# Kernel tuning notes

Measured on AMD Instinct MI355X. Metric: run time of the kernel, lower is better.

Reference implementation:

```python
import jax, jax.numpy as jnp
import numpy as np

N = 100000
E = 3200000
IN_C = 1433
DIM = 32
HEADS = 8
OUT_C = 4
NUM_LAYER = 2
NUM_CLASS = 7
NEG_SLOPE = 0.2


def setup_inputs() -> dict:
    key = jax.random.key(0)
    ks = jax.random.split(key, 12)
    s = 0.05
    return {
        "x": jax.random.normal(ks[0], (N, IN_C), dtype=jnp.float32),
        "edge_index": jax.random.randint(ks[1], (2, E), 0, N, dtype=jnp.int32),
        "w_proj": jax.random.normal(ks[2], (IN_C, DIM), dtype=jnp.float32) * s,
        "b_proj": jnp.zeros((DIM,), dtype=jnp.float32),
        "w_l": jax.random.normal(ks[3], (NUM_LAYER, DIM, HEADS * OUT_C), dtype=jnp.float32) * s,
        "b_l": jnp.zeros((NUM_LAYER, HEADS * OUT_C), dtype=jnp.float32),
        "w_r": jax.random.normal(ks[4], (NUM_LAYER, DIM, HEADS * OUT_C), dtype=jnp.float32) * s,
        "b_r": jnp.zeros((NUM_LAYER, HEADS * OUT_C), dtype=jnp.float32),
        "att": jax.random.normal(ks[5], (NUM_LAYER, HEADS, OUT_C), dtype=jnp.float32) * s,
        "conv_bias": jnp.zeros((NUM_LAYER, HEADS * OUT_C), dtype=jnp.float32),
        "w_pred": jax.random.normal(ks[6], (DIM, NUM_CLASS), dtype=jnp.float32) * s,
        "b_pred": jnp.zeros((NUM_CLASS,), dtype=jnp.float32),
    }


def _gatv2_layer(h, src, dst, wl, bl, wr, br, att, bias):
    # GATv2 (PyG semantics): x_l from source, x_r from target,
    # e = att . leaky_relu(x_l[src] + x_r[dst]); softmax over edges per dst.
    xl = (h @ wl + bl).reshape(N, HEADS, OUT_C)
    xr = (h @ wr + br).reshape(N, HEADS, OUT_C)
    e = jax.nn.leaky_relu(xl[src] + xr[dst], NEG_SLOPE)          # [E, H, C]
    logits = jnp.einsum("ehc,hc->eh", e, att)                    # [E, H]
    m = jax.ops.segment_max(logits, dst, num_segments=N)         # [N, H]
    m = jnp.where(jnp.isfinite(m), m, 0.0)                       # empty segments
    ex = jnp.exp(logits - m[dst])                                # [E, H]
    denom = jax.ops.segment_sum(ex, dst, num_segments=N)         # [N, H]
    alpha = ex / jnp.maximum(denom[dst], 1e-16)                  # [E, H]
    msg = alpha[:, :, None] * xl[src]                            # [E, H, C]
    out = jax.ops.segment_sum(msg, dst, num_segments=N)          # [N, H, C]
    return out.reshape(N, HEADS * OUT_C) + bias


def reference(x, edge_index, w_proj, b_proj, w_l, b_l, w_r, b_r, att, conv_bias, w_pred, b_pred):
    src = edge_index[0]
    dst = edge_index[1]
    h = x @ w_proj + b_proj                                      # [N, DIM]
    for i in range(NUM_LAYER):
        h = h + _gatv2_layer(h, src, dst, w_l[i], b_l[i], w_r[i], b_r[i], att[i], conv_bias[i])
    return h @ w_pred + b_pred                                   # [N, NUM_CLASS]
```

## Files before the change

kernel.cpp:

```cpp
#include <hip/hip_runtime.h>

#define N_NODES 100000
#define N_EDGES 3200000
#define IN_C 1433
#define DIM 32
#define HEADS 8
#define OUT_C 4
#define NUM_CLASS 7

#define KTILES 45
#define N_WAVES 6250
#define PROJ_BLOCKS 1563
#define NB_SCAN 98

typedef __bf16 bf16x8 __attribute__((ext_vector_type(8)));
typedef __bf16 bf16x4 __attribute__((ext_vector_type(4)));
typedef float f32x4 __attribute__((ext_vector_type(4)));

__global__ __launch_bounds__(256) void init_kernel(
    const float* __restrict__ w, const float* __restrict__ wl0,
    const float* __restrict__ wr0,
    bf16x8* __restrict__ wfrag, bf16x8* __restrict__ wfrag2,
    int* __restrict__ cnt) {
  const int g = blockIdx.x * 256 + threadIdx.x;
  if (g < N_NODES) cnt[g] = 0;
  if (blockIdx.x < KTILES * 2 && threadIdx.x < 64) {
    const int kt = blockIdx.x >> 1;
    const int ch = blockIdx.x & 1;
    const int l = threadIdx.x;
    const int col = ch * 16 + (l & 15);
    const int kbase = kt * 32 + (l >> 4) * 8;
    bf16x8 v;
    #pragma unroll
    for (int e = 0; e < 8; ++e) {
      const int k = kbase + e;
      v[e] = (__bf16)((k < IN_C) ? w[(size_t)k * DIM + col] : 0.f);
    }
    wfrag[(size_t)blockIdx.x * 64 + l] = v;
  } else if (blockIdx.x < KTILES * 2 + 4 && threadIdx.x < 64) {
    const int bf = blockIdx.x - KTILES * 2;
    const float* ws = (bf < 2) ? wl0 : wr0;
    const int ch = bf & 1;
    const int l = threadIdx.x;
    const int col = ch * 16 + (l & 15);
    const int kbase = (l >> 4) * 8;
    bf16x8 v;
    #pragma unroll
    for (int e = 0; e < 8; ++e)
      v[e] = (__bf16)ws[(size_t)(kbase + e) * DIM + col];
    wfrag2[(size_t)bf * 64 + l] = v;
  }
}

__global__ __launch_bounds__(256) void proj_count_kernel(
    const float* __restrict__ x, const bf16x8* __restrict__ wfrag,
    const bf16x8* __restrict__ wfrag2,
    const float* __restrict__ b, const float* __restrict__ bl0,
    const float* __restrict__ br0, float* __restrict__ h,
    __bf16* __restrict__ xlbA, float* __restrict__ xrA,
    const int* __restrict__ dst, int* __restrict__ cnt,
    int* __restrict__ rank) {
  __shared__ float stage[4][16 * 32];
  const int t = threadIdx.x;
  const int lane = t & 63;
  const int wid = t >> 6;
  const int widx = blockIdx.x * 4 + wid;

  if (widx < N_WAVES) {
    const int nodeBase = widx * 16;
    float* slab = stage[wid];

    const int qrow = lane >> 3;
    const int qcol = lane & 7;
    const float* xq = x + (size_t)(nodeBase + qrow) * IN_C + qcol * 4;

    const int frow = lane & 15;
    const int kg = lane >> 4;
    const int sw = frow & 7;
    const int rd0 = frow * 32 + (((2 * kg) ^ sw) << 2);
    const int rd1 = frow * 32 + (((2 * kg + 1) ^ sw) << 2);
    const bf16x8* wp = wfrag + lane;

    f32x4 acc0 = {0.f, 0.f, 0.f, 0.f};
    f32x4 acc1 = {0.f, 0.f, 0.f, 0.f};

    f32x4 a0 = *(const f32x4*)(xq);
    f32x4 b0v = *(const f32x4*)(xq + (size_t)8 * IN_C);
    f32x4 a1 = *(const f32x4*)(xq + 32);
    f32x4 b1v = *(const f32x4*)(xq + 32 + (size_t)8 * IN_C);

    for (int kt = 0; kt < KTILES - 1; ++kt) {
      {
        const int g0 = qcol ^ (qrow & 7);
        *(f32x4*)(slab + qrow * 32 + (g0 << 2)) = a0;
        const int r1 = qrow + 8;
        const int g1 = qcol ^ (r1 & 7);
        *(f32x4*)(slab + r1 * 32 + (g1 << 2)) = b0v;
      }
      a0 = a1; b0v = b1v;
      if (kt + 2 < KTILES - 1) {
        const float* xp = xq + (size_t)(kt + 2) * 32;
        a1 = *(const f32x4*)(xp);
        b1v = *(const f32x4*)(xp + (size_t)8 * IN_C);
      }
      const f32x4 lo = *(const f32x4*)(slab + rd0);
      const f32x4 hi = *(const f32x4*)(slab + rd1);
      bf16x8 af;
      af[0] = (__bf16)lo[0]; af[1] = (__bf16)lo[1];
      af[2] = (__bf16)lo[2]; af[3] = (__bf16)lo[3];
      af[4] = (__bf16)hi[0]; af[5] = (__bf16)hi[1];
      af[6] = (__bf16)hi[2]; af[7] = (__bf16)hi[3];
      const bf16x8 b0 = wp[(kt * 2 + 0) * 64];
      const bf16x8 b1 = wp[(kt * 2 + 1) * 64];
      acc0 = __builtin_amdgcn_mfma_f32_16x16x32_bf16(af, b0, acc0, 0, 0, 0);
      acc1 = __builtin_amdgcn_mfma_f32_16x16x32_bf16(af, b1, acc1, 0, 0, 0);
    }
    {
      const int srow = lane >> 5;
      const int scol = lane & 31;
      const bool ok = (1408 + scol) < IN_C;
      const float* xt = x + (size_t)(nodeBase + srow) * IN_C + 1408 + scol;
      #pragma unroll
      for (int i = 0; i < 8; ++i) {
        const int row = 2 * i + srow;
        const float v = ok ? xt[(size_t)(2 * i) * IN_C] : 0.f;
        const int p = (scol >> 2) ^ (row & 7);
        slab[row * 32 + (p << 2) + (scol & 3)] = v;
      }
      const f32x4 lo = *(const f32x4*)(slab + rd0);
      const f32x4 hi = *(const f32x4*)(slab + rd1);
      bf16x8 af;
      af[0] = (__bf16)lo[0]; af[1] = (__bf16)lo[1];
      af[2] = (__bf16)lo[2]; af[3] = (__bf16)lo[3];
      af[4] = (__bf16)hi[0]; af[5] = (__bf16)hi[1];
      af[6] = (__bf16)hi[2]; af[7] = (__bf16)hi[3];
      const bf16x8 b0 = wp[((KTILES - 1) * 2 + 0) * 64];
      const bf16x8 b1 = wp[((KTILES - 1) * 2 + 1) * 64];
      acc0 = __builtin_amdgcn_mfma_f32_16x16x32_bf16(af, b0, acc0, 0, 0, 0);
      acc1 = __builtin_amdgcn_mfma_f32_16x16x32_bf16(af, b1, acc1, 0, 0, 0);
    }

    const float bc0 = b[frow];
    const float bc1 = b[frow + 16];
    #pragma unroll
    for (int rg = 0; rg < 4; ++rg) {
      const int nl = kg * 4 + rg;
      const float o0 = acc0[rg] + bc0;
      const float o1 = acc1[rg] + bc1;
      const size_t o = (size_t)(nodeBase + nl) * DIM + frow;
      h[o] = o0;
      h[o + 16] = o1;
      slab[nl * 32 + frow] = o0;
      slab[nl * 32 + frow + 16] = o1;
    }
    {
      const f32x4 lo = *(const f32x4*)(slab + frow * 32 + kg * 8);
      const f32x4 hi = *(const f32x4*)(slab + frow * 32 + kg * 8 + 4);
      bf16x8 af;
      af[0] = (__bf16)lo[0]; af[1] = (__bf16)lo[1];
      af[2] = (__bf16)lo[2]; af[3] = (__bf16)lo[3];
      af[4] = (__bf16)hi[0]; af[5] = (__bf16)hi[1];
      af[6] = (__bf16)hi[2]; af[7] = (__bf16)hi[3];
      f32x4 xl0 = {0.f, 0.f, 0.f, 0.f}, xl1 = {0.f, 0.f, 0.f, 0.f};
      f32x4 xr0 = {0.f, 0.f, 0.f, 0.f}, xr1 = {0.f, 0.f, 0.f, 0.f};
      xl0 = __builtin_amdgcn_mfma_f32_16x16x32_bf16(af, wfrag2[0 * 64 + lane], xl0, 0, 0, 0);
      xl1 = __builtin_amdgcn_mfma_f32_16x16x32_bf16(af, wfrag2[1 * 64 + lane], xl1, 0, 0, 0);
      xr0 = __builtin_amdgcn_mfma_f32_16x16x32_bf16(af, wfrag2[2 * 64 + lane], xr0, 0, 0, 0);
      xr1 = __builtin_amdgcn_mfma_f32_16x16x32_bf16(af, wfrag2[3 * 64 + lane], xr1, 0, 0, 0);
      const float bl_0 = bl0[frow], bl_1 = bl0[frow + 16];
      const float br_0 = br0[frow], br_1 = br0[frow + 16];
      #pragma unroll
      for (int rg = 0; rg < 4; ++rg) {
        const int nl = kg * 4 + rg;
        const size_t o = ((size_t)(nodeBase + nl) << 5) + frow;
        xlbA[o] = (__bf16)(xl0[rg] + bl_0);
        xlbA[o + 16] = (__bf16)(xl1[rg] + bl_1);
        xrA[o] = xr0[rg] + br_0;
        xrA[o + 16] = xr1[rg] + br_1;
      }
    }
  }

  for (int e = blockIdx.x * 256 + t; e < N_EDGES; e += PROJ_BLOCKS * 256)
    rank[e] = atomicAdd(&cnt[dst[e]], 1);
}

__global__ __launch_bounds__(1024) void scan_local_kernel(
    const int* __restrict__ cnt, int* __restrict__ offs, int* __restrict__ bsum) {
  __shared__ int wsum[16];
  const int t = threadIdx.x;
  const int lane = t & 63;
  const int wid = t >> 6;
  const int idx = blockIdx.x * 1024 + t;
  const int v = (idx < N_NODES) ? cnt[idx] : 0;
  int incl = v;
  #pragma unroll
  for (int off = 1; off < 64; off <<= 1) {
    const int nv = __shfl_up(incl, off, 64);
    if (lane >= off) incl += nv;
  }
  if (lane == 63) wsum[wid] = incl;
  __syncthreads();
  int wpre = 0;
  for (int i = 0; i < wid; ++i) wpre += wsum[i];
  if (idx < N_NODES) offs[idx] = wpre + incl - v;
  if (t == 1023) bsum[blockIdx.x] = wpre + incl;
}

__global__ __launch_bounds__(256) void scan_add_kernel(
    int* __restrict__ offs, const int* __restrict__ bsum) {
  __shared__ int wsum[4];
  const int t = threadIdx.x;
  const int lane = t & 63;
  const int wid = t >> 6;
  const int k = blockIdx.x >> 2;
  int v = (t < k) ? bsum[t] : 0;
  #pragma unroll
  for (int m = 1; m < 64; m <<= 1) v += __shfl_xor(v, m, 64);
  if (lane == 0) wsum[wid] = v;
  __syncthreads();
  const int base = wsum[0] + wsum[1] + wsum[2] + wsum[3];
  const int idx = blockIdx.x * 256 + t;
  if (idx < N_NODES) offs[idx] += base;
  if (idx == 0) offs[N_NODES] = N_EDGES;
}

__global__ __launch_bounds__(256) void scatter_kernel(
    const int* __restrict__ src, const int* __restrict__ dst,
    const int* __restrict__ offs, const int* __restrict__ rank,
    int* __restrict__ srcs) {
  const int i = blockIdx.x * 256 + threadIdx.x;
  if (i < N_EDGES) {
    const int d = dst[i];
    srcs[offs[d] + rank[i]] = src[i];
  }
}

__global__ __launch_bounds__(256) void gat_lgemm_kernel(
    const float* __restrict__ hin, const __bf16* __restrict__ xlb,
    const float* __restrict__ xr, const float* __restrict__ att,
    const float* __restrict__ cbias, const int* __restrict__ offs,
    const int* __restrict__ srcs, float* __restrict__ hout,
    const float* __restrict__ wl1, const float* __restrict__ bl1,
    const float* __restrict__ wr1, const float* __restrict__ br1,
    __bf16* __restrict__ xlbB, float* __restrict__ xrB) {
  __shared__ float wls[DIM * DIM];
  __shared__ float wrs[DIM * DIM];
  const int t = threadIdx.x;
  for (int i2 = t; i2 < DIM * DIM; i2 += 256) { wls[i2] = wl1[i2]; wrs[i2] = wr1[i2]; }
  __syncthreads();

  const int lane = t & 63;
  const int node = blockIdx.x * 4 + (t >> 6);
  const int head = lane & 7;
  const int e8 = lane >> 3;
  const float4 a4 = *(const float4*)(att + head * 4);
  const float4 r4 = *(const float4*)(xr + (size_t)node * DIM + head * 4);
  const int beg = offs[node];
  const int end = offs[node + 1];
  float den = 0.f, acc0 = 0.f, acc1 = 0.f, acc2 = 0.f, acc3 = 0.f;
  int i = beg + e8;
  int sNext = (i < end) ? srcs[i] : 0;
  for (; i < end; i += 8) {
    const int s = sNext;
    if (i + 8 < end) sNext = srcs[i + 8];
    const bf16x4 lb = *(const bf16x4*)(xlb + ((size_t)s << 5) + (head << 2));
    const float l0 = (float)lb[0], l1 = (float)lb[1], l2 = (float)lb[2], l3 = (float)lb[3];
    float e0 = l0 + r4.x; e0 = (e0 > 0.f) ? e0 : 0.2f * e0;
    float e1 = l1 + r4.y; e1 = (e1 > 0.f) ? e1 : 0.2f * e1;
    float e2 = l2 + r4.z; e2 = (e2 > 0.f) ? e2 : 0.2f * e2;
    float e3 = l3 + r4.w; e3 = (e3 > 0.f) ? e3 : 0.2f * e3;
    const float logit = e0 * a4.x + e1 * a4.y + e2 * a4.z + e3 * a4.w;
    const float wgt = __expf(logit);
    den += wgt;
    acc0 += wgt * l0; acc1 += wgt * l1; acc2 += wgt * l2; acc3 += wgt * l3;
  }
  #pragma unroll
  for (int m = 8; m <= 32; m <<= 1) {
    den  += __shfl_xor(den, m, 64);
    acc0 += __shfl_xor(acc0, m, 64);
    acc1 += __shfl_xor(acc1, m, 64);
    acc2 += __shfl_xor(acc2, m, 64);
    acc3 += __shfl_xor(acc3, m, 64);
  }
  const float inv = 1.f / fmaxf(den, 1e-16f);
  const int o = node * DIM + head * 4;
  const float4 hv = *(const float4*)(hin + o);
  const float4 cb = *(const float4*)(cbias + head * 4);
  const float o0 = hv.x + cb.x + acc0 * inv;
  const float o1 = hv.y + cb.y + acc1 * inv;
  const float o2 = hv.z + cb.z + acc2 * inv;
  const float o3 = hv.w + cb.w + acc3 * inv;
  if (lane < 8) {
    float4 outv; outv.x = o0; outv.y = o1; outv.z = o2; outv.w = o3;
    *(float4*)(hout + o) = outv;
  }
  const int col = lane & 31;
  const float* wsel = (lane < 32) ? wls : wrs;
  float a = (lane < 32) ? bl1[col] : br1[col];
  #pragma unroll
  for (int k = 0; k < DIM; ++k) {
    const float src = (k & 3) == 0 ? o0 : (k & 3) == 1 ? o1 : (k & 3) == 2 ? o2 : o3;
    const float hk = __shfl(src, k >> 2, 64);
    a += hk * wsel[k * DIM + col];
  }
  const size_t xo = ((size_t)node << 5) + col;
  if (lane < 32) xlbB[xo] = (__bf16)a;
  else           xrB[xo] = a;
}

__global__ __launch_bounds__(256) void gat_edge_pred_kernel(
    const float* __restrict__ hin, const __bf16* __restrict__ xlb,
    const float* __restrict__ xr, const float* __restrict__ att,
    const float* __restrict__ cbias, const int* __restrict__ offs,
    const int* __restrict__ srcs,
    const float* __restrict__ wp, const float* __restrict__ bp,
    float* __restrict__ out) {
  const int t = threadIdx.x;
  const int lane = t & 63;
  const int node = blockIdx.x * 4 + (t >> 6);
  const int head = lane & 7;
  const int e8 = lane >> 3;
  const float4 a4 = *(const float4*)(att + head * 4);
  const float4 r4 = *(const float4*)(xr + (size_t)node * DIM + head * 4);
  const int beg = offs[node];
  const int end = offs[node + 1];
  float den = 0.f, acc0 = 0.f, acc1 = 0.f, acc2 = 0.f, acc3 = 0.f;
  int i = beg + e8;
  int sNext = (i < end) ? srcs[i] : 0;
  for (; i < end; i += 8) {
    const int s = sNext;
    if (i + 8 < end) sNext = srcs[i + 8];
    const bf16x4 lb = *(const bf16x4*)(xlb + ((size_t)s << 5) + (head << 2));
    const float l0 = (float)lb[0], l1 = (float)lb[1], l2 = (float)lb[2], l3 = (float)lb[3];
    float e0 = l0 + r4.x; e0 = (e0 > 0.f) ? e0 : 0.2f * e0;
    float e1 = l1 + r4.y; e1 = (e1 > 0.f) ? e1 : 0.2f * e1;
    float e2 = l2 + r4.z; e2 = (e2 > 0.f) ? e2 : 0.2f * e2;
    float e3 = l3 + r4.w; e3 = (e3 > 0.f) ? e3 : 0.2f * e3;
    const float logit = e0 * a4.x + e1 * a4.y + e2 * a4.z + e3 * a4.w;
    const float wgt = __expf(logit);
    den += wgt;
    acc0 += wgt * l0; acc1 += wgt * l1; acc2 += wgt * l2; acc3 += wgt * l3;
  }
  #pragma unroll
  for (int m = 8; m <= 32; m <<= 1) {
    den  += __shfl_xor(den, m, 64);
    acc0 += __shfl_xor(acc0, m, 64);
    acc1 += __shfl_xor(acc1, m, 64);
    acc2 += __shfl_xor(acc2, m, 64);
    acc3 += __shfl_xor(acc3, m, 64);
  }
  const float inv = 1.f / fmaxf(den, 1e-16f);
  const int o = node * DIM + head * 4;
  const float4 hv = *(const float4*)(hin + o);
  const float4 cb = *(const float4*)(cbias + head * 4);
  const float o0 = hv.x + cb.x + acc0 * inv;
  const float o1 = hv.y + cb.y + acc1 * inv;
  const float o2 = hv.z + cb.z + acc2 * inv;
  const float o3 = hv.w + cb.w + acc3 * inv;
  float pj[NUM_CLASS];
  const float* wr0 = wp + (head * 4 + 0) * NUM_CLASS;
  const float* wr1 = wp + (head * 4 + 1) * NUM_CLASS;
  const float* wr2 = wp + (head * 4 + 2) * NUM_CLASS;
  const float* wr3 = wp + (head * 4 + 3) * NUM_CLASS;
  #pragma unroll
  for (int j = 0; j < NUM_CLASS; ++j)
    pj[j] = o0 * wr0[j] + o1 * wr1[j] + o2 * wr2[j] + o3 * wr3[j];
  #pragma unroll
  for (int m = 1; m <= 4; m <<= 1) {
    #pragma unroll
    for (int j = 0; j < NUM_CLASS; ++j) pj[j] += __shfl_xor(pj[j], m, 64);
  }
  if (lane == 0) {
    #pragma unroll
    for (int j = 0; j < NUM_CLASS; ++j)
      out[(size_t)node * NUM_CLASS + j] = pj[j] + bp[j];
  }
}

extern "C" void kernel_launch(void* const* d_in, const int* in_sizes, int n_in,
                              void* d_out, int out_size, void* d_ws, size_t ws_size,
                              hipStream_t stream) {
  const float* x       = (const float*)d_in[0];
  const int*   ei      = (const int*)d_in[1];
  const float* w_proj  = (const float*)d_in[2];
  const float* b_proj  = (const float*)d_in[3];
  const float* w_l     = (const float*)d_in[4];
  const float* b_l     = (const float*)d_in[5];
  const float* w_r     = (const float*)d_in[6];
  const float* b_r     = (const float*)d_in[7];
  const float* att     = (const float*)d_in[8];
  const float* cbias   = (const float*)d_in[9];
  const float* w_pred  = (const float*)d_in[10];
  const float* b_pred  = (const float*)d_in[11];

  const int* e_src = ei;
  const int* e_dst = ei + N_EDGES;

  char* wsp = (char*)d_ws;
  size_t off = 0;
  auto take = [&](size_t bytes) -> void* {
    void* p = wsp + off;
    off += (bytes + 255) & ~(size_t)255;
    return p;
  };
  float*  h0     = (float*)take((size_t)N_NODES * DIM * 4);
  float*  h1     = (float*)take((size_t)N_NODES * DIM * 4);
  __bf16* xlbA   = (__bf16*)take((size_t)N_NODES * DIM * 2);
  float*  xrA    = (float*)take((size_t)N_NODES * DIM * 4);
  __bf16* xlbB   = (__bf16*)take((size_t)N_NODES * DIM * 2);
  float*  xrB    = (float*)take((size_t)N_NODES * DIM * 4);
  int*    offs   = (int*)take((size_t)(N_NODES + 1) * 4);
  int*    cnt    = (int*)take((size_t)N_NODES * 4);
  int*    bsum   = (int*)take((size_t)NB_SCAN * 4);
  int*    srcs   = (int*)take((size_t)N_EDGES * 4);
  int*    rank   = (int*)take((size_t)N_EDGES * 4);
  bf16x8* wfrag  = (bf16x8*)take((size_t)KTILES * 2 * 64 * 16);
  bf16x8* wfrag2 = (bf16x8*)take((size_t)4 * 64 * 16);

  init_kernel<<<(N_NODES + 255) / 256, 256, 0, stream>>>(
      w_proj, w_l, w_r, wfrag, wfrag2, cnt);
  proj_count_kernel<<<PROJ_BLOCKS, 256, 0, stream>>>(
      x, wfrag, wfrag2, b_proj, b_l, b_r, h0, xlbA, xrA, e_dst, cnt, rank);
  scan_local_kernel<<<NB_SCAN, 1024, 0, stream>>>(cnt, offs, bsum);
  scan_add_kernel<<<(N_NODES + 255) / 256, 256, 0, stream>>>(offs, bsum);
  scatter_kernel<<<(N_EDGES + 255) / 256, 256, 0, stream>>>(
      e_src, e_dst, offs, rank, srcs);
  gat_lgemm_kernel<<<N_NODES / 4, 256, 0, stream>>>(
      h0, xlbA, xrA, att, cbias, offs, srcs, h1,
      w_l + DIM * DIM, b_l + DIM, w_r + DIM * DIM, b_r + DIM, xlbB, xrB);
  gat_edge_pred_kernel<<<N_NODES / 4, 256, 0, stream>>>(
      h1, xlbB, xrB, att + HEADS * OUT_C, cbias + DIM, offs, srcs,
      w_pred, b_pred, (float*)d_out);
}
```

Measured before the change: 507.3 us.

## Fuse scan-add into scatter kernel and unroll edge gather loop by two

Merges the scan block-offset add and the edge scatter into one launch. Scatter blocks recompute the block-prefix bases in shared memory and add them on the fly, while extra blocks write the finalized offsets to a separate buffer. This removes one kernel launch and the serial dependency between the two. The per-node attention loop now processes two edges per iteration with two gathers in flight to improve memory-level parallelism, using a mask on the second edge; this adds some register pressure.

```diff
diff --git a/kernel.cpp b/kernel.cpp
--- a/kernel.cpp
+++ b/kernel.cpp
@@ -12,6 +12,8 @@
 #define N_WAVES 6250
 #define PROJ_BLOCKS 1563
 #define NB_SCAN 98
+#define SCAT_BLOCKS 12500
+#define ADD_BLOCKS 391
 
 typedef __bf16 bf16x8 __attribute__((ext_vector_type(8)));
 typedef __bf16 bf16x4 __attribute__((ext_vector_type(4)));
@@ -207,34 +209,112 @@
   if (t == 1023) bsum[blockIdx.x] = wpre + incl;
 }
 
-__global__ __launch_bounds__(256) void scan_add_kernel(
-    int* __restrict__ offs, const int* __restrict__ bsum) {
-  __shared__ int wsum[4];
+__global__ __launch_bounds__(256) void scatter_add_kernel(
+    const int* __restrict__ src, const int* __restrict__ dst,
+    const int* __restrict__ offs, const int* __restrict__ rank,
+    const int* __restrict__ bsum, int* __restrict__ srcs,
+    int* __restrict__ offs2) {
   const int t = threadIdx.x;
   const int lane = t & 63;
-  const int wid = t >> 6;
-  const int k = blockIdx.x >> 2;
-  int v = (t < k) ? bsum[t] : 0;
-  #pragma unroll
-  for (int m = 1; m < 64; m <<= 1) v += __shfl_xor(v, m, 64);
-  if (lane == 0) wsum[wid] = v;
-  __syncthreads();
-  const int base = wsum[0] + wsum[1] + wsum[2] + wsum[3];
-  const int idx = blockIdx.x * 256 + t;
-  if (idx < N_NODES) offs[idx] += base;
-  if (idx == 0) offs[N_NODES] = N_EDGES;
-}
-
-__global__ __launch_bounds__(256) void scatter_kernel(
-    const int* __restrict__ src, const int* __restrict__ dst,
-    const int* __restrict__ offs, const int* __restrict__ rank,
-    int* __restrict__ srcs) {
-  const int i = blockIdx.x * 256 + threadIdx.x;
-  if (i < N_EDGES) {
-    const int d = dst[i];
-    srcs[offs[d] + rank[i]] = src[i];
-  }
-}
+  if (blockIdx.x < SCAT_BLOCKS) {
+    __shared__ int sbase[128];
+    __shared__ int wtot;
+    int v = 0, incl = 0;
+    if (t < 128) {
+      v = (t < NB_SCAN) ? bsum[t] : 0;
+      incl = v;
+      #pragma unroll
+      for (int off = 1; off < 64; off <<= 1) {
+        const int nv = __shfl_up(incl, off, 64);
+        if (lane >= off) incl += nv;
+      }
+    }
+    if (t == 63) wtot = incl;
+    __syncthreads();
+    if (t < 128) sbase[t] = incl - v + ((t >= 64) ? wtot : 0);
+    __syncthreads();
+    const int i = blockIdx.x * 256 + t;
+    if (i < N_EDGES) {
+      const int d = dst[i];
+      srcs[offs[d] + sbase[d >> 10] + rank[i]] = src[i];
+    }
+  } else {
+    __shared__ int wsum[4];
+    const int wid = t >> 6;
+    const int bb = blockIdx.x - SCAT_BLOCKS;
+    const int k = bb >> 2;
+    int v = (t < k) ? bsum[t] : 0;
+    #pragma unroll
+    for (int m = 1; m < 64; m <<= 1) v += __shfl_xor(v, m, 64);
+    if (lane == 0) wsum[wid] = v;
+    __syncthreads();
+    const int base = wsum[0] + wsum[1] + wsum[2] + wsum[3];
+    const int idx = bb * 256 + t;
+    if (idx < N_NODES) offs2[idx] = offs[idx] + base;
+    if (idx == 0) offs2[N_NODES] = N_EDGES;
+  }
+}
+
+#define GAT_LOOP                                                              \
+  const int lane = t & 63;                                                    \
+  const int node = blockIdx.x * 4 + (t >> 6);                                 \
+  const int head = lane & 7;                                                  \
+  const int e8 = lane >> 3;                                                   \
+  const float4 a4 = *(const float4*)(att + head * 4);                         \
+  const float4 r4 = *(const float4*)(xr + (size_t)node * DIM + head * 4);     \
+  const int beg = offs[node];                                                 \
+  const int end = offs[node + 1];                                             \
+  float den = 0.f, acc0 = 0.f, acc1 = 0.f, acc2 = 0.f, acc3 = 0.f;            \
+  int i = beg + e8;                                                           \
+  int s0 = (i < end) ? srcs[i] : 0;                                           \
+  int s1 = (i + 8 < end) ? srcs[i + 8] : 0;                                   \
+  for (; i < end; i += 16) {                                                  \
+    const float v1 = (i + 8 < end) ? 1.f : 0.f;                               \
+    const bf16x4 lbA = *(const bf16x4*)(xlb + ((size_t)s0 << 5) + (head << 2));\
+    const bf16x4 lbB = *(const bf16x4*)(xlb + ((size_t)s1 << 5) + (head << 2));\
+    const int j = i + 16;                                                     \
+    s0 = (j < end) ? srcs[j] : 0;                                             \
+    s1 = (j + 8 < end) ? srcs[j + 8] : 0;                                     \
+    {                                                                         \
+      const float l0 = (float)lbA[0], l1 = (float)lbA[1];                     \
+      const float l2 = (float)lbA[2], l3 = (float)lbA[3];                     \
+      float e0 = l0 + r4.x; e0 = (e0 > 0.f) ? e0 : 0.2f * e0;                 \
+      float e1 = l1 + r4.y; e1 = (e1 > 0.f) ? e1 : 0.2f * e1;                 \
+      float e2 = l2 + r4.z; e2 = (e2 > 0.f) ? e2 : 0.2f * e2;                 \
+      float e3 = l3 + r4.w; e3 = (e3 > 0.f) ? e3 : 0.2f * e3;                 \
+      const float wgt = __expf(e0 * a4.x + e1 * a4.y + e2 * a4.z + e3 * a4.w);\
+      den += wgt;                                                             \
+      acc0 += wgt * l0; acc1 += wgt * l1; acc2 += wgt * l2; acc3 += wgt * l3; \
+    }                                                                         \
+    {                                                                         \
+      const float l0 = (float)lbB[0], l1 = (float)lbB[1];                     \
+      const float l2 = (float)lbB[2], l3 = (float)lbB[3];                     \
+      float e0 = l0 + r4.x; e0 = (e0 > 0.f) ? e0 : 0.2f * e0;                 \
+      float e1 = l1 + r4.y; e1 = (e1 > 0.f) ? e1 : 0.2f * e1;                 \
+      float e2 = l2 + r4.z; e2 = (e2 > 0.f) ? e2 : 0.2f * e2;                 \
+      float e3 = l3 + r4.w; e3 = (e3 > 0.f) ? e3 : 0.2f * e3;                 \
+      const float wgt =                                                       \
+          v1 * __expf(e0 * a4.x + e1 * a4.y + e2 * a4.z + e3 * a4.w);         \
+      den += wgt;                                                             \
+      acc0 += wgt * l0; acc1 += wgt * l1; acc2 += wgt * l2; acc3 += wgt * l3; \
+    }                                                                         \
+  }                                                                           \
+  _Pragma("unroll")                                                           \
+  for (int m = 8; m <= 32; m <<= 1) {                                         \
+    den  += __shfl_xor(den, m, 64);                                           \
+    acc0 += __shfl_xor(acc0, m, 64);                                          \
+    acc1 += __shfl_xor(acc1, m, 64);                                          \
+    acc2 += __shfl_xor(acc2, m, 64);                                          \
+    acc3 += __shfl_xor(acc3, m, 64);                                          \
+  }                                                                           \
+  const float inv = 1.f / fmaxf(den, 1e-16f);                                 \
+  const int o = node * DIM + head * 4;                                        \
+  const float4 hv = *(const float4*)(hin + o);                                \
+  const float4 cb = *(const float4*)(cbias + head * 4);                       \
+  const float o0 = hv.x + cb.x + acc0 * inv;                                  \
+  const float o1 = hv.y + cb.y + acc1 * inv;                                  \
+  const float o2 = hv.z + cb.z + acc2 * inv;                                  \
+  const float o3 = hv.w + cb.w + acc3 * inv;
 
 __global__ __launch_bounds__(256) void gat_lgemm_kernel(
     const float* __restrict__ hin, const __bf16* __restrict__ xlb,
@@ -250,47 +330,8 @@
   for (int i2 = t; i2 < DIM * DIM; i2 += 256) { wls[i2] = wl1[i2]; wrs[i2] = wr1[i2]; }
   __syncthreads();
 
-  const int lane = t & 63;
-  const int node = blockIdx.x * 4 + (t >> 6);
-  const int head = lane & 7;
-  const int e8 = lane >> 3;
-  const float4 a4 = *(const float4*)(att + head * 4);
-  const float4 r4 = *(const float4*)(xr + (size_t)node * DIM + head * 4);
-  const int beg = offs[node];
-  const int end = offs[node + 1];
-  float den = 0.f, acc0 = 0.f, acc1 = 0.f, acc2 = 0.f, acc3 = 0.f;
-  int i = beg + e8;
-  int sNext = (i < end) ? srcs[i] : 0;
-  for (; i < end; i += 8) {
-    const int s = sNext;
-    if (i + 8 < end) sNext = srcs[i + 8];
-    const bf16x4 lb = *(const bf16x4*)(xlb + ((size_t)s << 5) + (head << 2));
-    const float l0 = (float)lb[0], l1 = (float)lb[1], l2 = (float)lb[2], l3 = (float)lb[3];
-    float e0 = l0 + r4.x; e0 = (e0 > 0.f) ? e0 : 0.2f * e0;
-    float e1 = l1 + r4.y; e1 = (e1 > 0.f) ? e1 : 0.2f * e1;
-    float e2 = l2 + r4.z; e2 = (e2 > 0.f) ? e2 : 0.2f * e2;
-    float e3 = l3 + r4.w; e3 = (e3 > 0.f) ? e3 : 0.2f * e3;
-    const float logit = e0 * a4.x + e1 * a4.y + e2 * a4.z + e3 * a4.w;
-    const float wgt = __expf(logit);
-    den += wgt;
-    acc0 += wgt * l0; acc1 += wgt * l1; acc2 += wgt * l2; acc3 += wgt * l3;
-  }
-  #pragma unroll
-  for (int m = 8; m <= 32; m <<= 1) {
-    den  += __shfl_xor(den, m, 64);
-    acc0 += __shfl_xor(acc0, m, 64);
-    acc1 += __shfl_xor(acc1, m, 64);
-    acc2 += __shfl_xor(acc2, m, 64);
-    acc3 += __shfl_xor(acc3, m, 64);
-  }
-  const float inv = 1.f / fmaxf(den, 1e-16f);
-  const int o = node * DIM + head * 4;
-  const float4 hv = *(const float4*)(hin + o);
-  const float4 cb = *(const float4*)(cbias + head * 4);
-  const float o0 = hv.x + cb.x + acc0 * inv;
-  const float o1 = hv.y + cb.y + acc1 * inv;
-  const float o2 = hv.z + cb.z + acc2 * inv;
-  const float o3 = hv.w + cb.w + acc3 * inv;
+  GAT_LOOP
+
   if (lane < 8) {
     float4 outv; outv.x = o0; outv.y = o1; outv.z = o2; outv.w = o3;
     *(float4*)(hout + o) = outv;
@@ -317,47 +358,9 @@
     const float* __restrict__ wp, const float* __restrict__ bp,
     float* __restrict__ out) {
   const int t = threadIdx.x;
-  const int lane = t & 63;
-  const int node = blockIdx.x * 4 + (t >> 6);
-  const int head = lane & 7;
-  const int e8 = lane >> 3;
-  const float4 a4 = *(const float4*)(att + head * 4);
-  const float4 r4 = *(const float4*)(xr + (size_t)node * DIM + head * 4);
-  const int beg = offs[node];
-  const int end = offs[node + 1];
-  float den = 0.f, acc0 = 0.f, acc1 = 0.f, acc2 = 0.f, acc3 = 0.f;
-  int i = beg + e8;
-  int sNext = (i < end) ? srcs[i] : 0;
-  for (; i < end; i += 8) {
-    const int s = sNext;
-    if (i + 8 < end) sNext = srcs[i + 8];
-    const bf16x4 lb = *(const bf16x4*)(xlb + ((size_t)s << 5) + (head << 2));
-    const float l0 = (float)lb[0], l1 = (float)lb[1], l2 = (float)lb[2], l3 = (float)lb[3];
-    float e0 = l0 + r4.x; e0 = (e0 > 0.f) ? e0 : 0.2f * e0;
-    float e1 = l1 + r4.y; e1 = (e1 > 0.f) ? e1 : 0.2f * e1;
-    float e2 = l2 + r4.z; e2 = (e2 > 0.f) ? e2 : 0.2f * e2;
-    float e3 = l3 + r4.w; e3 = (e3 > 0.f) ? e3 : 0.2f * e3;
-    const float logit = e0 * a4.x + e1 * a4.y + e2 * a4.z + e3 * a4.w;
-    const float wgt = __expf(logit);
-    den += wgt;
-    acc0 += wgt * l0; acc1 += wgt * l1; acc2 += wgt * l2; acc3 += wgt * l3;
-  }
-  #pragma unroll
-  for (int m = 8; m <= 32; m <<= 1) {
-    den  += __shfl_xor(den, m, 64);
-    acc0 += __shfl_xor(acc0, m, 64);
-    acc1 += __shfl_xor(acc1, m, 64);
-    acc2 += __shfl_xor(acc2, m, 64);
-    acc3 += __shfl_xor(acc3, m, 64);
-  }
-  const float inv = 1.f / fmaxf(den, 1e-16f);
-  const int o = node * DIM + head * 4;
-  const float4 hv = *(const float4*)(hin + o);
-  const float4 cb = *(const float4*)(cbias + head * 4);
-  const float o0 = hv.x + cb.x + acc0 * inv;
-  const float o1 = hv.y + cb.y + acc1 * inv;
-  const float o2 = hv.z + cb.z + acc2 * inv;
-  const float o3 = hv.w + cb.w + acc3 * inv;
+
+  GAT_LOOP
+
   float pj[NUM_CLASS];
   const float* wr0 = wp + (head * 4 + 0) * NUM_CLASS;
   const float* wr1 = wp + (head * 4 + 1) * NUM_CLASS;
@@ -411,6 +414,7 @@
   __bf16* xlbB   = (__bf16*)take((size_t)N_NODES * DIM * 2);
   float*  xrB    = (float*)take((size_t)N_NODES * DIM * 4);
   int*    offs   = (int*)take((size_t)(N_NODES + 1) * 4);
+  int*    offs2  = (int*)take((size_t)(N_NODES + 1) * 4);
   int*    cnt    = (int*)take((size_t)N_NODES * 4);
   int*    bsum   = (int*)take((size_t)NB_SCAN * 4);
   int*    srcs   = (int*)take((size_t)N_EDGES * 4);
@@ -423,13 +427,12 @@
   proj_count_kernel<<<PROJ_BLOCKS, 256, 0, stream>>>(
       x, wfrag, wfrag2, b_proj, b_l, b_r, h0, xlbA, xrA, e_dst, cnt, rank);
   scan_local_kernel<<<NB_SCAN, 1024, 0, stream>>>(cnt, offs, bsum);
-  scan_add_kernel<<<(N_NODES + 255) / 256, 256, 0, stream>>>(offs, bsum);
-  scatter_kernel<<<(N_EDGES + 255) / 256, 256, 0, stream>>>(
-      e_src, e_dst, offs, rank, srcs);
+  scatter_add_kernel<<<SCAT_BLOCKS + ADD_BLOCKS, 256, 0, stream>>>(
+      e_src, e_dst, offs, rank, bsum, srcs, offs2);
   gat_lgemm_kernel<<<N_NODES / 4, 256, 0, stream>>>(
-      h0, xlbA, xrA, att, cbias, offs, srcs, h1,
+      h0, xlbA, xrA, att, cbias, offs2, srcs, h1,
       w_l + DIM * DIM, b_l + DIM, w_r + DIM * DIM, b_r + DIM, xlbB, xrB);
   gat_edge_pred_kernel<<<N_NODES / 4, 256, 0, stream>>>(
-      h1, xlbB, xrB, att + HEADS * OUT_C, cbias + DIM, offs, srcs,
+      h1, xlbB, xrB, att + HEADS * OUT_C, cbias + DIM, offs2, srcs,
       w_pred, b_pred, (float*)d_out);
 }
```

Result: no change. 498.0 us (-1.8%).
